# Optimization experiments

Hardware: AMD Instinct MI355X
Metric: run time of the kernel (lower is better)

The kernel has to match this reference:

```python
import jax, jax.numpy as jnp
import numpy as np

H_SVD_MEDIUM_20 = np.array([+0.3279, +1.0, -0.9373, -0.8584, +0.6153, -0.5127, -0.3207, +0.8355,
                            -0.7528, +0.6792, +0.5284, -0.8558, -0.4101, -0.7967, -0.6088, -0.5275,
                            -0.2591, +0.894, +0.0663, +0.1645], dtype=np.float32)

def _inv_softplus(y, eps=1e-8):
    y = float(max(y, eps))
    return float(np.log(np.expm1(y)))

def setup_inputs() -> dict:
    key = jax.random.key(0)
    k1, k2, k3 = jax.random.split(key, 3)
    B, L, K, NUM_AA = 32, 8192, 64, 20
    seq = jax.random.randint(k1, (B, L), 0, NUM_AA, dtype=jnp.int64 if jax.config.jax_enable_x64 else jnp.int32)
    r = jax.random.uniform(k2, (B, L, K), dtype=jnp.float32) * 15.0
    j_idx = jax.random.randint(k3, (B, L, K), 0, L, dtype=seq.dtype)
    h = jnp.asarray(H_SVD_MEDIUM_20)                      # learned pair vector, SVD init
    r_half_raw = jnp.float32(_inv_softplus(6.5))
    tau_hp_raw = jnp.float32(_inv_softplus(1.5))
    return {"seq": seq, "r": r, "j_idx": j_idx, "h": h,
            "r_half_raw": r_half_raw, "tau_hp_raw": tau_hp_raw, "max_dist": 10}

def reference(seq, r, j_idx, h, r_half_raw, tau_hp_raw, max_dist):
    B, L, K = r.shape
    md = jnp.float32(max_dist)
    r_peak = jax.nn.softplus(r_half_raw)
    sigma = jax.nn.softplus(tau_hp_raw) + 0.1
    valid = (r < md - 1e-4).astype(r.dtype)               # [B,L,K]
    h_i = h[seq]                                          # [B,L]
    j_safe = jnp.clip(j_idx, 0, L - 1)
    seq_j = jnp.take_along_axis(seq, j_safe.reshape(B, L * K), axis=1).reshape(B, L, K)
    h_j = h[seq_j]                                        # [B,L,K]
    r_c = jnp.minimum(r, md)
    g = jnp.exp(-(r_c - r_peak) ** 2 / (2.0 * sigma ** 2)) * valid
    E_hp_i = jnp.sum(h_i[..., None] * h_j * g, axis=-1)   # [B,L]
    return E_hp_i
```

## Files before the change

kernel.cpp:

```cpp
#include <hip/hip_runtime.h>


#define BB 32
#define LL 8192
#define KK 64

__global__ __launch_bounds__(256) void _HydrophobicPairs_58256936403302_kernel(
    const int*   __restrict__ seq,
    const float* __restrict__ r,
    const int*   __restrict__ j_idx,
    const float* __restrict__ h,
    const float* __restrict__ r_half_raw,
    const float* __restrict__ tau_hp_raw,
    const int*   __restrict__ max_dist,
    float*       __restrict__ out)
{
    __shared__ float lds_h[20];
    const int tid = threadIdx.x;
    if (tid < 20) lds_h[tid] = h[tid];
    __syncthreads();

    const float md     = (float)max_dist[0];
    const float r_peak = log1pf(expf(r_half_raw[0]));
    const float sigma  = log1pf(expf(tau_hp_raw[0])) + 0.1f;
    const float inv2s2 = 1.0f / (2.0f * sigma * sigma);
    const float vthr   = md - 1e-4f;

    const int row  = blockIdx.x * 16 + (tid >> 4);
    const int lane = tid & 15;
    const int* seq_b = seq + (row & ~(LL - 1));

    const long base = (long)row * KK + lane * 4;
    const float4 r4 = *(const float4*)(r + base);
    const int4   j4 = *(const int4*)(j_idx + base);

    float acc = 0.0f;
    #pragma unroll
    for (int t = 0; t < 4; ++t) {
        const float rv = (&r4.x)[t];
        int j = (&j4.x)[t];
        j = min(max(j, 0), LL - 1);
        const float hj = lds_h[seq_b[j]];
        const float rc = fminf(rv, md);
        const float d  = rc - r_peak;
        float g = __expf(-d * d * inv2s2);
        g = (rv < vthr) ? g : 0.0f;
        acc = fmaf(hj, g, acc);
    }

    acc += __shfl_xor(acc, 1);
    acc += __shfl_xor(acc, 2);
    acc += __shfl_xor(acc, 4);
    acc += __shfl_xor(acc, 8);

    if (lane == 0) {
        const float hi = lds_h[seq[row]];
        out[row] = hi * acc;
    }
}

extern "C" void kernel_launch(void* const* d_in, const int* in_sizes, int n_in,
                              void* d_out, int out_size, void* d_ws, size_t ws_size,
                              hipStream_t stream) {
    const int*   seq        = (const int*)d_in[0];
    const float* r          = (const float*)d_in[1];
    const int*   j_idx      = (const int*)d_in[2];
    const float* h          = (const float*)d_in[3];
    const float* r_half_raw = (const float*)d_in[4];
    const float* tau_hp_raw = (const float*)d_in[5];
    const int*   max_dist   = (const int*)d_in[6];
    float*       out        = (float*)d_out;

    const int rows = BB * LL;
    dim3 grid(rows / 16), block(256);
    _HydrophobicPairs_58256936403302_kernel<<<grid, block, 0, stream>>>(
        seq, r, j_idx, h, r_half_raw, tau_hp_raw, max_dist, out);
}
```

Before: 184.5 us.

## Stage per-batch h[seq] row in LDS and process multiple rows per thread

Each block first builds an 8192-entry table of h[seq] for its batch in shared memory. The random neighbour gather then reads that LDS table, replacing the dependent global seq load followed by an LDS lookup. Blocks are enlarged to 1024 threads covering 512 rows, and each thread handles 16 neighbours across two rows with wide vector loads, which puts more memory requests in flight. The exponential is rewritten as exp2f with a folded scale, and the index clamp becomes a bitmask. The costs are redundant seq loads per block (16 blocks per batch), 32KB of LDS per block limiting occupancy, and a grid of only 512 large blocks.

```diff
diff --git a/kernel.cpp b/kernel.cpp
--- a/kernel.cpp
+++ b/kernel.cpp
@@ -4,8 +4,10 @@
 #define BB 32
 #define LL 8192
 #define KK 64
+#define TPB 1024
+#define ROWS_PER_BLOCK 512
 
-__global__ __launch_bounds__(256) void _HydrophobicPairs_58256936403302_kernel(
+__global__ __launch_bounds__(TPB) void _HydrophobicPairs_58256936403302_kernel(
     const int*   __restrict__ seq,
     const float* __restrict__ r,
     const int*   __restrict__ j_idx,
@@ -15,47 +17,66 @@
     const int*   __restrict__ max_dist,
     float*       __restrict__ out)
 {
-    __shared__ float lds_h[20];
+    __shared__ float h_row[LL];
+    __shared__ float h_tab[32];
+
     const int tid = threadIdx.x;
-    if (tid < 20) lds_h[tid] = h[tid];
+    if (tid < 20) h_tab[tid] = h[tid];
     __syncthreads();
+
+    const int chunk = blockIdx.x & 15;
+    const int b     = blockIdx.x >> 4;
+    const int lbase = chunk * ROWS_PER_BLOCK;
+
+    const int4* seq4 = (const int4*)(seq + b * LL);
+    #pragma unroll
+    for (int i = 0; i < 2; ++i) {
+        const int idx = tid + i * TPB;
+        const int4 s = seq4[idx];
+        const float4 hv = make_float4(h_tab[s.x], h_tab[s.y], h_tab[s.z], h_tab[s.w]);
+        ((float4*)h_row)[idx] = hv;
+    }
 
     const float md     = (float)max_dist[0];
     const float r_peak = log1pf(expf(r_half_raw[0]));
     const float sigma  = log1pf(expf(tau_hp_raw[0])) + 0.1f;
-    const float inv2s2 = 1.0f / (2.0f * sigma * sigma);
+    const float nscale = -1.44269504f / (2.0f * sigma * sigma);
     const float vthr   = md - 1e-4f;
 
-    const int row  = blockIdx.x * 16 + (tid >> 4);
-    const int lane = tid & 15;
-    const int* seq_b = seq + (row & ~(LL - 1));
+    __syncthreads();
 
-    const long base = (long)row * KK + lane * 4;
-    const float4 r4 = *(const float4*)(r + base);
-    const int4   j4 = *(const int4*)(j_idx + base);
+    const int lane = tid & 3;
+    #pragma unroll
+    for (int o = 0; o < 2; ++o) {
+        const int l_loc = lbase + o * 256 + (tid >> 2);
+        const int row   = b * LL + l_loc;
+        const long base = (long)row * KK + lane * 16;
 
-    float acc = 0.0f;
-    #pragma unroll
-    for (int t = 0; t < 4; ++t) {
-        const float rv = (&r4.x)[t];
-        int j = (&j4.x)[t];
-        j = min(max(j, 0), LL - 1);
-        const float hj = lds_h[seq_b[j]];
-        const float rc = fminf(rv, md);
-        const float d  = rc - r_peak;
-        float g = __expf(-d * d * inv2s2);
-        g = (rv < vthr) ? g : 0.0f;
-        acc = fmaf(hj, g, acc);
-    }
+        float4 r4[4]; int4 j4[4];
+        #pragma unroll
+        for (int t = 0; t < 4; ++t) {
+            r4[t] = *(const float4*)(r + base + t * 4);
+            j4[t] = *(const int4*)(j_idx + base + t * 4);
+        }
 
-    acc += __shfl_xor(acc, 1);
-    acc += __shfl_xor(acc, 2);
-    acc += __shfl_xor(acc, 4);
-    acc += __shfl_xor(acc, 8);
+        float acc = 0.0f;
+        #pragma unroll
+        for (int t = 0; t < 4; ++t) {
+            #pragma unroll
+            for (int u = 0; u < 4; ++u) {
+                const float rv = (&r4[t].x)[u];
+                const unsigned j = (unsigned)(&j4[t].x)[u] & (LL - 1);
+                const float hj = h_row[j];
+                const float d  = fminf(rv, md) - r_peak;
+                float g = exp2f(d * d * nscale);
+                g = (rv < vthr) ? g : 0.0f;
+                acc = fmaf(hj, g, acc);
+            }
+        }
 
-    if (lane == 0) {
-        const float hi = lds_h[seq[row]];
-        out[row] = hi * acc;
+        acc += __shfl_xor(acc, 1);
+        acc += __shfl_xor(acc, 2);
+        if (lane == 0) out[row] = h_row[l_loc] * acc;
     }
 }
 
@@ -71,8 +92,7 @@
     const int*   max_dist   = (const int*)d_in[6];
     float*       out        = (float*)d_out;
 
-    const int rows = BB * LL;
-    dim3 grid(rows / 16), block(256);
+    dim3 grid(BB * (LL / ROWS_PER_BLOCK)), block(TPB);
     _HydrophobicPairs_58256936403302_kernel<<<grid, block, 0, stream>>>(
         seq, r, j_idx, h, r_half_raw, tau_hp_raw, max_dist, out);
 }
```

Result: faster. 160.6 us (-13.0%).

## Stage per-batch h[seq] row in LDS and gather neighbours from shared memory

Applied to the files above, without the earlier changes.

A small pre-kernel computes h[seq] for all positions into workspace. The main kernel then has each block load its batch's full 8192-entry h row into LDS, and gathers neighbour values with an LDS lookup instead of a random global seq read followed by an LDS h lookup. Each block now handles 256 rows with 512 threads, prefetching the next r/j_idx vectors in software, and uses exp2f with a prescaled constant. The cost is an extra launch, 32KB of LDS per block that limits occupancy, and masking j instead of clamping it, which gives different results for out-of-range indices.

```diff
diff --git a/kernel.cpp b/kernel.cpp
--- a/kernel.cpp
+++ b/kernel.cpp
@@ -4,58 +4,86 @@
 #define BB 32
 #define LL 8192
 #define KK 64
+#define TPB 512
+#define RPB 256
 
-__global__ __launch_bounds__(256) void _HydrophobicPairs_58256936403302_kernel(
-    const int*   __restrict__ seq,
+__global__ __launch_bounds__(256) void _hp_hall_kernel(
+    const int* __restrict__ seq, const float* __restrict__ h,
+    float* __restrict__ h_all)
+{
+    const int idx = blockIdx.x * 256 + threadIdx.x;
+    const int4 s = ((const int4*)seq)[idx];
+    ((float4*)h_all)[idx] = make_float4(h[s.x], h[s.y], h[s.z], h[s.w]);
+}
+
+__global__ __launch_bounds__(TPB) void _HydrophobicPairs_58256936403302_kernel(
     const float* __restrict__ r,
     const int*   __restrict__ j_idx,
-    const float* __restrict__ h,
+    const float* __restrict__ h_all,
     const float* __restrict__ r_half_raw,
     const float* __restrict__ tau_hp_raw,
     const int*   __restrict__ max_dist,
     float*       __restrict__ out)
 {
-    __shared__ float lds_h[20];
-    const int tid = threadIdx.x;
-    if (tid < 20) lds_h[tid] = h[tid];
-    __syncthreads();
+    __shared__ float h_row[LL];
+    const int tid   = threadIdx.x;
+    const int b     = blockIdx.x >> 5;
+    const int chunk = blockIdx.x & 31;
+    const int lbase = chunk * RPB;
+
+    const float4* hsrc = (const float4*)(h_all + b * LL);
+    #pragma unroll
+    for (int i = 0; i < 4; ++i) {
+        const int e4 = i * TPB + tid;
+        ((float4*)h_row)[e4] = hsrc[e4];
+    }
 
     const float md     = (float)max_dist[0];
     const float r_peak = log1pf(expf(r_half_raw[0]));
     const float sigma  = log1pf(expf(tau_hp_raw[0])) + 0.1f;
-    const float inv2s2 = 1.0f / (2.0f * sigma * sigma);
+    const float nscale = -1.44269504f / (2.0f * sigma * sigma);
     const float vthr   = md - 1e-4f;
 
-    const int row  = blockIdx.x * 16 + (tid >> 4);
     const int lane = tid & 15;
-    const int* seq_b = seq + (row & ~(LL - 1));
+    const int rgrp = tid >> 4;
+    const long base0 = ((long)(b * LL + lbase + rgrp)) * KK + lane * 4;
 
-    const long base = (long)row * KK + lane * 4;
-    const float4 r4 = *(const float4*)(r + base);
-    const int4   j4 = *(const int4*)(j_idx + base);
+    float4 rv = *(const float4*)(r + base0);
+    int4   jv = *(const int4*)(j_idx + base0);
 
-    float acc = 0.0f;
+    __syncthreads();
+
     #pragma unroll
-    for (int t = 0; t < 4; ++t) {
-        const float rv = (&r4.x)[t];
-        int j = (&j4.x)[t];
-        j = min(max(j, 0), LL - 1);
-        const float hj = lds_h[seq_b[j]];
-        const float rc = fminf(rv, md);
-        const float d  = rc - r_peak;
-        float g = __expf(-d * d * inv2s2);
-        g = (rv < vthr) ? g : 0.0f;
-        acc = fmaf(hj, g, acc);
-    }
+    for (int it = 0; it < 8; ++it) {
+        const float4 rc = rv;
+        const int4   jc = jv;
+        if (it < 7) {
+            const long nb = base0 + (long)(it + 1) * (32 * KK);
+            rv = *(const float4*)(r + nb);
+            jv = *(const int4*)(j_idx + nb);
+        }
 
-    acc += __shfl_xor(acc, 1);
-    acc += __shfl_xor(acc, 2);
-    acc += __shfl_xor(acc, 4);
-    acc += __shfl_xor(acc, 8);
+        float acc = 0.0f;
+        #pragma unroll
+        for (int u = 0; u < 4; ++u) {
+            const float rvv = (&rc.x)[u];
+            const unsigned j = (unsigned)(&jc.x)[u] & (LL - 1);
+            const float hj = h_row[j];
+            const float d  = fminf(rvv, md) - r_peak;
+            float g = exp2f(d * d * nscale);
+            g = (rvv < vthr) ? g : 0.0f;
+            acc = fmaf(hj, g, acc);
+        }
 
-    if (lane == 0) {
-        const float hi = lds_h[seq[row]];
-        out[row] = hi * acc;
+        acc += __shfl_xor(acc, 1);
+        acc += __shfl_xor(acc, 2);
+        acc += __shfl_xor(acc, 4);
+        acc += __shfl_xor(acc, 8);
+
+        if (lane == 0) {
+            const int l_loc = lbase + it * 32 + rgrp;
+            out[b * LL + l_loc] = h_row[l_loc] * acc;
+        }
     }
 }
 
@@ -70,9 +98,10 @@
     const float* tau_hp_raw = (const float*)d_in[5];
     const int*   max_dist   = (const int*)d_in[6];
     float*       out        = (float*)d_out;
+    float*       h_all      = (float*)d_ws;
 
-    const int rows = BB * LL;
-    dim3 grid(rows / 16), block(256);
-    _HydrophobicPairs_58256936403302_kernel<<<grid, block, 0, stream>>>(
-        seq, r, j_idx, h, r_half_raw, tau_hp_raw, max_dist, out);
+    _hp_hall_kernel<<<dim3(256), dim3(256), 0, stream>>>(seq, h, h_all);
+
+    _HydrophobicPairs_58256936403302_kernel<<<dim3(BB * (LL / RPB)), dim3(TPB), 0, stream>>>(
+        r, j_idx, h_all, r_half_raw, tau_hp_raw, max_dist, out);
 }
```

After: 163.6 us. 1.13x faster.
